# Performance work log

Hardware: AMD Instinct MI355X
Metric: run time of the kernel (lower is better)

The kernel has to match this reference:

```python
import jax, jax.numpy as jnp
import numpy as np

B, L, D, H = 4, 1024, 1024, 16
DH = D // H


def setup_inputs() -> dict:
    key = jax.random.key(0)
    ks = jax.random.split(key, 10)
    x_embed = jax.random.normal(ks[0], (B, L, D), dtype=jnp.float32)
    bemb = jax.random.normal(ks[1], (B, L), dtype=jnp.float32)
    s = 0.02
    Wq_w = jax.random.normal(ks[2], (D, D), dtype=jnp.float32) * s
    Wk_w = jax.random.normal(ks[3], (D, D), dtype=jnp.float32) * s
    Wv_w = jax.random.normal(ks[4], (D, D), dtype=jnp.float32) * s
    Wo_w = jax.random.normal(ks[5], (D, D), dtype=jnp.float32) * s
    Wq_b = jnp.zeros((D,), jnp.float32)
    Wk_b = jnp.zeros((D,), jnp.float32)
    Wv_b = jnp.zeros((D,), jnp.float32)
    Wo_b = jnp.zeros((D,), jnp.float32)
    return dict(x_embed=x_embed, bemb=bemb, Wq_w=Wq_w, Wq_b=Wq_b,
                Wk_w=Wk_w, Wk_b=Wk_b, Wv_w=Wv_w, Wv_b=Wv_b,
                Wo_w=Wo_w, Wo_b=Wo_b)


def reference(x_embed, bemb, Wq_w, Wq_b, Wk_w, Wk_b, Wv_w, Wv_b, Wo_w, Wo_b):
    # present[b, l] = token l of batch b participates in attention
    present = bemb > 0  # [B, L]

    def proj(w, b):
        # torch Linear: y = x W^T + b; split heads -> [B, H, L, DH]
        y = jnp.einsum('bld,ed->ble', x_embed, w) + b
        return y.reshape(B, L, H, DH).transpose(0, 2, 1, 3)

    Q = proj(Wq_w, Wq_b)
    K = proj(Wk_w, Wk_b)
    V = proj(Wv_w, Wv_b)

    scores = jnp.einsum('bhqd,bhkd->bhqk', Q, K) / jnp.sqrt(jnp.float32(DH))
    # pre-softmax column mask: absent keys -> -inf
    scores = jnp.where(present[:, None, None, :], scores, -jnp.inf)
    A = jax.nn.softmax(scores, axis=-1)  # [B, H, L, L]
    # post-softmax row mask: subtract 1 on absent query rows, then relu
    row_absent = (~present).astype(A.dtype)[:, None, :, None]  # [B,1,L,1]
    A = jnp.maximum(A - row_absent, 0.0)

    out = jnp.einsum('bhqk,bhkd->bhqd', A, V)
    out = out.transpose(0, 2, 1, 3).reshape(B, L, D)
    out = jnp.einsum('bld,ed->ble', out, Wo_w) + Wo_b
    return out, A
```

## Files before the change

kernel.cpp:

```cpp
#include <hip/hip_runtime.h>
#include <math.h>

#define BB 4
#define LL 1024
#define DD 1024
#define HH 16
#define MROWS 4096

typedef __attribute__((ext_vector_type(8))) short short8;
typedef __attribute__((ext_vector_type(4))) float f32x4;
typedef __attribute__((ext_vector_type(4))) unsigned short us4;

__device__ inline unsigned short f2bf(float f) {
    unsigned int u = __builtin_bit_cast(unsigned int, f);
    u += 0x7fffu + ((u >> 16) & 1u);
    return (unsigned short)(u >> 16);
}

__device__ inline void gl2lds16(const void* g, void* l) {
    __builtin_amdgcn_global_load_lds(
        (const __attribute__((address_space(1))) void*)g,
        (__attribute__((address_space(3))) void*)l, 16, 0, 0);
}

__global__ __launch_bounds__(256) void cvt_all(const float* __restrict__ x,
                                               const float* __restrict__ wq,
                                               const float* __restrict__ wk,
                                               const float* __restrict__ wv,
                                               const float* __restrict__ wo,
                                               unsigned short* __restrict__ xb,
                                               unsigned short* __restrict__ wqb,
                                               unsigned short* __restrict__ wkb,
                                               unsigned short* __restrict__ wvb,
                                               unsigned short* __restrict__ wob) {
    int i = blockIdx.x * 256 + threadIdx.x;
    const float* src; unsigned short* dst; int k;
    if (i < 1048576) { src = x; dst = xb; k = i; }
    else {
        int j = i - 1048576; int w = j >> 18; k = j & 262143;
        src = (w == 0) ? wq : (w == 1) ? wk : (w == 2) ? wv : wo;
        dst = (w == 0) ? wqb : (w == 1) ? wkb : (w == 2) ? wvb : wob;
    }
    float4 v = ((const float4*)src)[k];
    us4 p = { f2bf(v.x), f2bf(v.y), f2bf(v.z), f2bf(v.w) };
    ((us4*)dst)[k] = p;
}

__device__ __forceinline__ void gemm_core(const unsigned short* __restrict__ X,
                                          const unsigned short* __restrict__ W,
                                          const float* __restrict__ bias,
                                          void* __restrict__ Cv, int out_mode) {
    __shared__ unsigned short SMEM[2][128][64];
    #define Xs SMEM[0]
    #define Ws SMEM[1]
    const int t = threadIdx.x;
    const int lane = t & 63, quad = lane >> 4, lm = lane & 15;
    const int wave = t >> 6;
    const int mo = (wave & 1) * 64, no = (wave >> 1) * 64;
    const int row0 = blockIdx.x * 128, col0 = blockIdx.y * 128;
    const int sw = lm & 7;

    const int r_in = lane >> 3;
    const int sg = (lane & 7) ^ r_in;
    const int lrow = wave * 32 + r_in;
    const unsigned short* xp = X + (size_t)(row0 + lrow) * 1024 + sg * 8;
    const unsigned short* wp = W + (size_t)(col0 + lrow) * 1024 + sg * 8;
    unsigned short* ldsX = &Xs[wave * 32][0];
    unsigned short* ldsW = &Ws[wave * 32][0];

    f32x4 acc[4][4] = {};

    for (int kc = 0; kc < 1024; kc += 64) {
        #pragma unroll
        for (int j = 0; j < 4; ++j) {
            gl2lds16(xp + (size_t)j * 8192 + kc, ldsX + j * 512);
            gl2lds16(wp + (size_t)j * 8192 + kc, ldsW + j * 512);
        }
        __syncthreads();
        #pragma unroll
        for (int s = 0; s < 2; ++s) {
            short8 af[4], bf[4];
            #pragma unroll
            for (int mi = 0; mi < 4; ++mi)
                af[mi] = *(const short8*)&Xs[mo + mi * 16 + lm][((s * 4 + quad) ^ sw) * 8];
            #pragma unroll
            for (int nj = 0; nj < 4; ++nj)
                bf[nj] = *(const short8*)&Ws[no + nj * 16 + lm][((s * 4 + quad) ^ sw) * 8];
            #pragma unroll
            for (int mi = 0; mi < 4; ++mi)
                #pragma unroll
                for (int nj = 0; nj < 4; ++nj)
                    acc[mi][nj] = __builtin_amdgcn_mfma_f32_16x16x32_bf16(
                        af[mi], bf[nj], acc[mi][nj], 0, 0, 0);
        }
        __syncthreads();
    }

    if (out_mode == 2) {
        unsigned short* Ct = &SMEM[0][0][0];
        #pragma unroll
        for (int mi = 0; mi < 4; ++mi) {
            #pragma unroll
            for (int nj = 0; nj < 4; ++nj) {
                int ccol = no + nj * 16 + lm;
                int crow0 = mo + mi * 16 + quad * 4;
                float bv = bias[col0 + ccol];
                us4 pk = { f2bf(acc[mi][nj][0] + bv), f2bf(acc[mi][nj][1] + bv),
                           f2bf(acc[mi][nj][2] + bv), f2bf(acc[mi][nj][3] + bv) };
                *(us4*)&Ct[ccol * 128 + (crow0 ^ ((ccol & 15) << 3))] = pk;
            }
        }
        __syncthreads();
        const int b = row0 >> 10, l0c = row0 & 1023;
        #pragma unroll
        for (int it = 0; it < 8; ++it) {
            int cc = (t >> 4) + it * 16;
            int lb = (t & 15) * 8;
            short8 v = *(const short8*)&Ct[cc * 128 + (lb ^ ((cc & 15) << 3))];
            int gcol = col0 + cc;
            int hh = gcol >> 6, dd = gcol & 63;
            *(short8*)&((unsigned short*)Cv)[(((size_t)b * 16 + hh) * 64 + dd) * 1024 + l0c + lb] = v;
        }
        return;
    }

    #pragma unroll
    for (int mi = 0; mi < 4; ++mi) {
        #pragma unroll
        for (int nj = 0; nj < 4; ++nj) {
            int gr0 = row0 + mo + mi * 16 + quad * 4;
            int gc  = col0 + no + nj * 16 + lm;
            float bv = bias[gc];
            #pragma unroll
            for (int r = 0; r < 4; ++r) {
                float val = acc[mi][nj][r] + bv;
                int gr = gr0 + r;
                if (out_mode == 0) {
                    __builtin_nontemporal_store(val, &((float*)Cv)[(size_t)gr * 1024 + gc]);
                } else {
                    ((unsigned short*)Cv)[(size_t)gr * 1024 + gc] = f2bf(val);
                }
            }
        }
    }
    #undef Xs
    #undef Ws
}

__global__ __launch_bounds__(256) void qkv_proj(const unsigned short* __restrict__ xb,
                                                const unsigned short* __restrict__ wq,
                                                const unsigned short* __restrict__ wk,
                                                const unsigned short* __restrict__ wv,
                                                const float* __restrict__ bq,
                                                const float* __restrict__ bk,
                                                const float* __restrict__ bv,
                                                unsigned short* __restrict__ Qw,
                                                unsigned short* __restrict__ Kw,
                                                unsigned short* __restrict__ Vt) {
    const int z = blockIdx.z;
    const unsigned short* W = (z == 0) ? wq : (z == 1) ? wk : wv;
    const float* b = (z == 0) ? bq : (z == 1) ? bk : bv;
    void* C = (z == 0) ? (void*)Qw : (z == 1) ? (void*)Kw : (void*)Vt;
    gemm_core(xb, W, b, C, (z == 2) ? 2 : 1);
}

__global__ __launch_bounds__(256) void out_proj(const unsigned short* __restrict__ Aw,
                                                const unsigned short* __restrict__ wo,
                                                const float* __restrict__ bo,
                                                float* __restrict__ out) {
    gemm_core(Aw, wo, bo, out, 0);
}

__global__ __launch_bounds__(512) void attn_fused(const unsigned short* __restrict__ Qw,
                                                  const unsigned short* __restrict__ Kw,
                                                  const unsigned short* __restrict__ Vt,
                                                  const float* __restrict__ bemb,
                                                  float* __restrict__ Aout,
                                                  unsigned short* __restrict__ attn) {
    __shared__ unsigned short Ks[128][64];
    __shared__ unsigned short Vs[64][128];
    __shared__ unsigned short Ps[8][16][132];
    __shared__ float maskadd[1024];
    const int t = threadIdx.x;
    const int lane = t & 63, quad = lane >> 4, lm = lane & 15;
    const int w = t >> 6;
    const int q0 = blockIdx.x * 128;
    const int bh = blockIdx.y;
    const int b = bh >> 4, h = bh & 15;
    const int qrow_frag = q0 + w * 16 + lm;
    const int qrow_acc0 = q0 + w * 16 + quad * 4;
    const int swk = lm & 7;

    const int kr_in = lane >> 3;
    const int ksg = (lane & 7) ^ kr_in;
    const unsigned short* kp = Kw + (size_t)(b * 1024 + w * 16 + kr_in) * 1024 + h * 64 + ksg * 8;
    unsigned short* ldsK = &Ks[w * 16][0];
    const int vr_in = lane >> 4, vcg = lane & 15;
    const int vrow = w * 8 + vr_in;
    const unsigned short* vpbase = Vt + (size_t)bh * 64 * 1024;
    unsigned short* ldsV = &Vs[w * 8][0];

    for (int i = t; i < 1024; i += 512)
        maskadd[i] = (bemb[b * 1024 + i] > 0.f) ? 0.f : -1e30f;

    short8 afq[2];
    #pragma unroll
    for (int s = 0; s < 2; ++s)
        afq[s] = *(const short8*)&Qw[(size_t)(b * 1024 + qrow_frag) * 1024 +
                                     h * 64 + s * 32 + quad * 8];

    float lsum[4] = { 0.f, 0.f, 0.f, 0.f };

    __syncthreads();

    for (int c = 0; c < 8; ++c) {
        #pragma unroll
        for (int j = 0; j < 2; ++j)
            gl2lds16(kp + (size_t)(c * 128 + j * 8) * 1024, ldsK + j * 512);
        __syncthreads();

        f32x4 acc[8] = {};
        #pragma unroll
        for (int s = 0; s < 2; ++s)
            #pragma unroll
            for (int nj = 0; nj < 8; ++nj) {
                short8 bfk = *(const short8*)&Ks[nj * 16 + lm][((s * 4 + quad) ^ swk) * 8];
                acc[nj] = __builtin_amdgcn_mfma_f32_16x16x32_bf16(afq[s], bfk, acc[nj], 0, 0, 0);
            }

        #pragma unroll
        for (int nj = 0; nj < 8; ++nj) {
            float ma = maskadd[c * 128 + nj * 16 + lm];
            #pragma unroll
            for (int r = 0; r < 4; ++r)
                lsum[r] += __expf(acc[nj][r] * 0.125f + ma);
        }
        __syncthreads();
    }

    float fnorm[4];
    #pragma unroll
    for (int r = 0; r < 4; ++r) {
        float s = lsum[r];
        #pragma unroll
        for (int off = 8; off >= 1; off >>= 1)
            s += __shfl_xor(s, off, 64);
        bool qp = bemb[b * 1024 + qrow_acc0 + r] > 0.f;
        fnorm[r] = (qp && s > 0.f) ? (1.f / s) : 0.f;
    }

    f32x4 oacc[4] = {};
    for (int c = 0; c < 8; ++c) {
        #pragma unroll
        for (int j = 0; j < 2; ++j) {
            gl2lds16(kp + (size_t)(c * 128 + j * 8) * 1024, ldsK + j * 512);
            int rl = vrow + j * 4;
            int vsg = vcg ^ (rl & 15);
            gl2lds16(vpbase + (size_t)rl * 1024 + c * 128 + vsg * 8, ldsV + j * 512);
        }
        __syncthreads();

        f32x4 acc[8] = {};
        #pragma unroll
        for (int s = 0; s < 2; ++s)
            #pragma unroll
            for (int nj = 0; nj < 8; ++nj) {
                short8 bfk = *(const short8*)&Ks[nj * 16 + lm][((s * 4 + quad) ^ swk) * 8];
                acc[nj] = __builtin_amdgcn_mfma_f32_16x16x32_bf16(afq[s], bfk, acc[nj], 0, 0, 0);
            }

        #pragma unroll
        for (int nj = 0; nj < 8; ++nj) {
            float ma = maskadd[c * 128 + nj * 16 + lm];
            #pragma unroll
            for (int r = 0; r < 4; ++r) {
                float p  = __expf(acc[nj][r] * 0.125f + ma);
                float a  = p * fnorm[r];
                __builtin_nontemporal_store(
                    a, &Aout[((size_t)bh * 1024 + qrow_acc0 + r) * 1024 + c * 128 + nj * 16 + lm]);
                Ps[w][quad * 4 + r][nj * 16 + lm] = f2bf(a);
            }
        }

        #pragma unroll
        for (int ks = 0; ks < 4; ++ks) {
            short8 afp = *(const short8*)&Ps[w][lm][ks * 32 + quad * 8];
            #pragma unroll
            for (int nd = 0; nd < 4; ++nd) {
                short8 bfv = *(const short8*)&Vs[nd * 16 + lm][((ks * 4 + quad) ^ lm) * 8];
                oacc[nd] = __builtin_amdgcn_mfma_f32_16x16x32_bf16(afp, bfv, oacc[nd], 0, 0, 0);
            }
        }
        __syncthreads();
    }

    #pragma unroll
    for (int nd = 0; nd < 4; ++nd)
        #pragma unroll
        for (int r = 0; r < 4; ++r)
            attn[(size_t)(b * 1024 + qrow_acc0 + r) * 1024 + h * 64 + nd * 16 + lm] =
                f2bf(oacc[nd][r]);
}

extern "C" void kernel_launch(void* const* d_in, const int* in_sizes, int n_in,
                              void* d_out, int out_size, void* d_ws, size_t ws_size,
                              hipStream_t stream) {
    const float* x    = (const float*)d_in[0];
    const float* bemb = (const float*)d_in[1];
    const float* Wq   = (const float*)d_in[2];
    const float* Wq_b = (const float*)d_in[3];
    const float* Wk   = (const float*)d_in[4];
    const float* Wk_b = (const float*)d_in[5];
    const float* Wv   = (const float*)d_in[6];
    const float* Wv_b = (const float*)d_in[7];
    const float* Wo   = (const float*)d_in[8];
    const float* Wo_b = (const float*)d_in[9];

    float* out  = (float*)d_out;
    float* Aout = out + (size_t)BB * LL * DD;

    unsigned short* x_bf  = (unsigned short*)d_ws;
    unsigned short* Wq_bf = x_bf  + (size_t)MROWS * DD;
    unsigned short* Wk_bf = Wq_bf + (size_t)DD * DD;
    unsigned short* Wv_bf = Wk_bf + (size_t)DD * DD;
    unsigned short* Wo_bf = Wv_bf + (size_t)DD * DD;
    unsigned short* Qw    = Wo_bf + (size_t)DD * DD;
    unsigned short* Kw    = Qw + (size_t)MROWS * DD;
    unsigned short* Vt    = Kw + (size_t)MROWS * DD;
    unsigned short* Aw    = x_bf;

    cvt_all<<<dim3(8192), dim3(256), 0, stream>>>(x, Wq, Wk, Wv, Wo,
                                                  x_bf, Wq_bf, Wk_bf, Wv_bf, Wo_bf);

    qkv_proj<<<dim3(MROWS / 128, DD / 128, 3), dim3(256), 0, stream>>>(
        x_bf, Wq_bf, Wk_bf, Wv_bf, Wq_b, Wk_b, Wv_b, Qw, Kw, Vt);

    attn_fused<<<dim3(LL / 128, BB * HH), dim3(512), 0, stream>>>(
        Qw, Kw, Vt, bemb, Aout, Aw);

    out_proj<<<dim3(MROWS / 128, DD / 128), dim3(256), 0, stream>>>(
        Aw, Wo_bf, Wo_b, out);
}
```

Measured before the change: 451.2 us.

## Load K/V MFMA fragments directly from global, drop LDS staging and barriers

The attention kernel stops staging K and V tiles in shared memory through async global-to-LDS copies. Each wave now reads its MFMA B-fragments straight from global memory and relies on L1/L2 for reuse across the 8 waves, which removes the per-chunk __syncthreads barriers. Nontemporal stores for the attention matrix and the output projection become ordinary stores. The cost is eight times more global/L2 traffic for K and V, with each row read as scattered 16-byte pieces, and the large A output now passes through the cache.

New measurement: 548.2 us. +21.5%, slower.

```diff
diff --git a/kernel.cpp b/kernel.cpp
--- a/kernel.cpp
+++ b/kernel.cpp
@@ -136,7 +136,7 @@
                 float val = acc[mi][nj][r] + bv;
                 int gr = gr0 + r;
                 if (out_mode == 0) {
-                    __builtin_nontemporal_store(val, &((float*)Cv)[(size_t)gr * 1024 + gc]);
+                    ((float*)Cv)[(size_t)gr * 1024 + gc] = val;
                 } else {
                     ((unsigned short*)Cv)[(size_t)gr * 1024 + gc] = f2bf(val);
                 }
@@ -177,8 +177,6 @@
                                                   const float* __restrict__ bemb,
                                                   float* __restrict__ Aout,
                                                   unsigned short* __restrict__ attn) {
-    __shared__ unsigned short Ks[128][64];
-    __shared__ unsigned short Vs[64][128];
     __shared__ unsigned short Ps[8][16][132];
     __shared__ float maskadd[1024];
     const int t = threadIdx.x;
@@ -189,16 +187,6 @@
     const int b = bh >> 4, h = bh & 15;
     const int qrow_frag = q0 + w * 16 + lm;
     const int qrow_acc0 = q0 + w * 16 + quad * 4;
-    const int swk = lm & 7;
-
-    const int kr_in = lane >> 3;
-    const int ksg = (lane & 7) ^ kr_in;
-    const unsigned short* kp = Kw + (size_t)(b * 1024 + w * 16 + kr_in) * 1024 + h * 64 + ksg * 8;
-    unsigned short* ldsK = &Ks[w * 16][0];
-    const int vr_in = lane >> 4, vcg = lane & 15;
-    const int vrow = w * 8 + vr_in;
-    const unsigned short* vpbase = Vt + (size_t)bh * 64 * 1024;
-    unsigned short* ldsV = &Vs[w * 8][0];
 
     for (int i = t; i < 1024; i += 512)
         maskadd[i] = (bemb[b * 1024 + i] > 0.f) ? 0.f : -1e30f;
@@ -209,25 +197,22 @@
         afq[s] = *(const short8*)&Qw[(size_t)(b * 1024 + qrow_frag) * 1024 +
                                      h * 64 + s * 32 + quad * 8];
 
+    const unsigned short* kfrag = Kw + (size_t)(b * 1024 + lm) * 1024 + h * 64 + quad * 8;
+    const unsigned short* vfrag = Vt + ((size_t)bh * 64 + lm) * 1024 + quad * 8;
+
     float lsum[4] = { 0.f, 0.f, 0.f, 0.f };
 
     __syncthreads();
 
     for (int c = 0; c < 8; ++c) {
-        #pragma unroll
-        for (int j = 0; j < 2; ++j)
-            gl2lds16(kp + (size_t)(c * 128 + j * 8) * 1024, ldsK + j * 512);
-        __syncthreads();
-
         f32x4 acc[8] = {};
         #pragma unroll
         for (int s = 0; s < 2; ++s)
             #pragma unroll
             for (int nj = 0; nj < 8; ++nj) {
-                short8 bfk = *(const short8*)&Ks[nj * 16 + lm][((s * 4 + quad) ^ swk) * 8];
+                short8 bfk = *(const short8*)&kfrag[(size_t)(c * 128 + nj * 16) * 1024 + s * 32];
                 acc[nj] = __builtin_amdgcn_mfma_f32_16x16x32_bf16(afq[s], bfk, acc[nj], 0, 0, 0);
             }
-
         #pragma unroll
         for (int nj = 0; nj < 8; ++nj) {
             float ma = maskadd[c * 128 + nj * 16 + lm];
@@ -235,7 +220,6 @@
             for (int r = 0; r < 4; ++r)
                 lsum[r] += __expf(acc[nj][r] * 0.125f + ma);
         }
-        __syncthreads();
     }
 
     float fnorm[4];
@@ -251,21 +235,12 @@
 
     f32x4 oacc[4] = {};
     for (int c = 0; c < 8; ++c) {
-        #pragma unroll
-        for (int j = 0; j < 2; ++j) {
-            gl2lds16(kp + (size_t)(c * 128 + j * 8) * 1024, ldsK + j * 512);
-            int rl = vrow + j * 4;
-            int vsg = vcg ^ (rl & 15);
-            gl2lds16(vpbase + (size_t)rl * 1024 + c * 128 + vsg * 8, ldsV + j * 512);
-        }
-        __syncthreads();
-
         f32x4 acc[8] = {};
         #pragma unroll
         for (int s = 0; s < 2; ++s)
             #pragma unroll
             for (int nj = 0; nj < 8; ++nj) {
-                short8 bfk = *(const short8*)&Ks[nj * 16 + lm][((s * 4 + quad) ^ swk) * 8];
+                short8 bfk = *(const short8*)&kfrag[(size_t)(c * 128 + nj * 16) * 1024 + s * 32];
                 acc[nj] = __builtin_amdgcn_mfma_f32_16x16x32_bf16(afq[s], bfk, acc[nj], 0, 0, 0);
             }
 
@@ -276,8 +251,7 @@
             for (int r = 0; r < 4; ++r) {
                 float p  = __expf(acc[nj][r] * 0.125f + ma);
                 float a  = p * fnorm[r];
-                __builtin_nontemporal_store(
-                    a, &Aout[((size_t)bh * 1024 + qrow_acc0 + r) * 1024 + c * 128 + nj * 16 + lm]);
+                Aout[((size_t)bh * 1024 + qrow_acc0 + r) * 1024 + c * 128 + nj * 16 + lm] = a;
                 Ps[w][quad * 4 + r][nj * 16 + lm] = f2bf(a);
             }
         }
@@ -287,11 +261,10 @@
             short8 afp = *(const short8*)&Ps[w][lm][ks * 32 + quad * 8];
             #pragma unroll
             for (int nd = 0; nd < 4; ++nd) {
-                short8 bfv = *(const short8*)&Vs[nd * 16 + lm][((ks * 4 + quad) ^ lm) * 8];
+                short8 bfv = *(const short8*)&vfrag[(size_t)(nd * 16) * 1024 + c * 128 + ks * 32];
                 oacc[nd] = __builtin_amdgcn_mfma_f32_16x16x32_bf16(afp, bfv, oacc[nd], 0, 0, 0);
             }
         }
-        __syncthreads();
     }
 
     #pragma unroll
```
